# Kernel optimization log

Measured on AMD Instinct MI355X. Metric: run time of the kernel, lower is better.

## Reference

```python
import jax, jax.numpy as jnp
import numpy as np

EPS_SUM = 1e-8   # matches tf divide epsilon on column sums
EPS_L2 = 1e-12   # tf.nn.l2_normalize default epsilon inside CosineSimilarity
EPS_LOG = 1e-8


def _l2norm_rows(x):
    # rows: (k, N); matches tf.nn.l2_normalize(x, axis=-1)
    sq = jnp.sum(x * x, axis=-1, keepdims=True)
    return x * jax.lax.rsqrt(jnp.maximum(sq, EPS_L2))


def setup_inputs() -> dict:
    key = jax.random.key(0)
    k0, k1 = jax.random.split(key)
    N, K = 200000, 256
    c_0 = jax.random.uniform(k0, (N, K), dtype=jnp.float32)
    c_1 = jax.random.uniform(k1, (N, K), dtype=jnp.float32)
    return {"c_0": c_0, "c_1": c_1, "k": K}


def reference(c_0, c_1, k):
    # --- cluster-size entropy terms ---
    s0 = jnp.sum(c_0, axis=0)                      # (k,)
    s1 = jnp.sum(c_1, axis=0)
    p_0 = s0 / jnp.sum(s0)
    p_1 = s1 / jnp.sum(s1)
    log_k = jnp.log(jnp.float32(k))
    entrpy_loss = (jnp.sum(p_0 * jnp.log(p_0)) + log_k) + \
                  (jnp.sum(p_1 * jnp.log(p_1)) + log_k)

    # --- column-sum normalize, transpose to (k, N) ---
    c0n = (c_0 / (s0[None, :] + EPS_SUM)).T        # (k, N)
    c1n = (c_1 / (s1[None, :] + EPS_SUM)).T        # (k, N)

    # cosine similarity matrix via row L2-normalization + small GEMM
    a = _l2norm_rows(c0n)                          # (k, N)
    b = _l2norm_rows(c1n)                          # (k, N)
    c_smi = jnp.einsum('kn,jn->kj', a, b)          # (k, k) cosine sims

    diag = jnp.diagonal(jax.nn.softmax(c_smi, axis=-1))  # (k,)
    cls_loss = -jnp.mean(jnp.log(diag + EPS_LOG))
    return (cls_loss, entrpy_loss)
```

## Files before the change

kernel.cpp:

```cpp
#include <hip/hip_runtime.h>
#include <hip/hip_bf16.h>

typedef __attribute__((ext_vector_type(4))) float f32x4;
typedef __attribute__((ext_vector_type(4))) int   i32x4;
typedef __attribute__((ext_vector_type(8))) short s16x8;

#define KCOLS 256
#define KC 32

__device__ __forceinline__ unsigned int f2bf(float v){
    union { float f; unsigned int u; } x; x.f = v;
    return (x.u + 0x7fffu + ((x.u >> 16) & 1u)) >> 16;
}

__global__ __launch_bounds__(512, 2) void k1_gemm(
        const float* __restrict__ c0, const float* __restrict__ c1,
        float* __restrict__ Pc, float* __restrict__ Ps, int nrows)
{
    const int tid = threadIdx.x;
    const int w   = tid >> 6;
    const int l   = tid & 63;
    const int mat = w >> 2;
    const int oct = w & 3;
    const int wr  = w >> 2;
    const int wc  = w & 3;
    const int b   = blockIdx.x;
    const int B   = gridDim.x;
    const int nchunk = (nrows + KC - 1) / KC;

    __shared__ __align__(16) unsigned short lds[2][2][8192];
    __shared__ float sred[2][4][256];
    __shared__ float qred[2][4][256];

    const float* src = mat ? c1 : c0;
    const int colbase = l << 2;
    const int wsw = ((oct ^ (l & 3)) << 3);

    int idxA[8], idxB[4];
#pragma unroll
    for (int mt = 0; mt < 8; ++mt){
        int col = wr*128 + mt*16 + (l & 15);
        idxA[mt] = col*32 + ((((l >> 4)) ^ ((col >> 2) & 3)) << 3);
    }
#pragma unroll
    for (int nt = 0; nt < 4; ++nt){
        int col = wc*64 + nt*16 + (l & 15);
        idxB[nt] = col*32 + ((((l >> 4)) ^ ((col >> 2) & 3)) << 3);
    }

    f32x4 acc[8][4];
    const f32x4 zf = {0.f, 0.f, 0.f, 0.f};
#pragma unroll
    for (int i = 0; i < 8; ++i)
#pragma unroll
        for (int j = 0; j < 4; ++j) acc[i][j] = zf;

    float sum[4] = {0.f,0.f,0.f,0.f};
    float sq [4] = {0.f,0.f,0.f,0.f};

    f32x4 f[8];
    int c = b;
    if (c < nchunk){
        int rbase = c*KC + oct*8;
#pragma unroll
        for (int rr = 0; rr < 8; ++rr){
            int row = rbase + rr;
            f[rr] = (row < nrows) ? *(const f32x4*)(src + (size_t)row*KCOLS + colbase) : zf;
        }
    }

    int p = 0;
    while (c < nchunk){
        unsigned short* dst = &lds[p][mat][0];
#pragma unroll
        for (int cc = 0; cc < 4; ++cc){
            float v0=f[0][cc], v1=f[1][cc], v2=f[2][cc], v3=f[3][cc];
            float v4=f[4][cc], v5=f[5][cc], v6=f[6][cc], v7=f[7][cc];
            sum[cc] += ((v0+v1)+(v2+v3)) + ((v4+v5)+(v6+v7));
            sq [cc] += ((v0*v0+v1*v1)+(v2*v2+v3*v3)) + ((v4*v4+v5*v5)+(v6*v6+v7*v7));
            i32x4 pk;
            pk.x = (int)(f2bf(v0) | (f2bf(v1) << 16));
            pk.y = (int)(f2bf(v2) | (f2bf(v3) << 16));
            pk.z = (int)(f2bf(v4) | (f2bf(v5) << 16));
            pk.w = (int)(f2bf(v6) | (f2bf(v7) << 16));
            *(i32x4*)&dst[(colbase + cc)*32 + wsw] = pk;
        }
        __syncthreads();

        int cn = c + B;
        if (cn < nchunk){
            int rbase = cn*KC + oct*8;
#pragma unroll
            for (int rr = 0; rr < 8; ++rr){
                int row = rbase + rr;
                f[rr] = (row < nrows) ? *(const f32x4*)(src + (size_t)row*KCOLS + colbase) : zf;
            }
        }

        const unsigned short* bufA = &lds[p][0][0];
        const unsigned short* bufB = &lds[p][1][0];
        s16x8 bfr[4];
#pragma unroll
        for (int nt = 0; nt < 4; ++nt) bfr[nt] = *(const s16x8*)&bufB[idxB[nt]];
#pragma unroll
        for (int mt = 0; mt < 8; ++mt){
            s16x8 afr = *(const s16x8*)&bufA[idxA[mt]];
#pragma unroll
            for (int nt = 0; nt < 4; ++nt)
                acc[mt][nt] = __builtin_amdgcn_mfma_f32_16x16x32_bf16(
                                  afr, bfr[nt], acc[mt][nt], 0, 0, 0);
        }
        p ^= 1;
        c  = cn;
    }

    float* Pb = Pc + (size_t)b * 65536;
#pragma unroll
    for (int mt = 0; mt < 8; ++mt)
#pragma unroll
        for (int nt = 0; nt < 4; ++nt)
#pragma unroll
            for (int r = 0; r < 4; ++r){
                int row = wr*128 + mt*16 + (l >> 4)*4 + r;
                int cl  = wc*64  + nt*16 + (l & 15);
                Pb[row*256 + cl] = acc[mt][nt][r];
            }

#pragma unroll
    for (int cc = 0; cc < 4; ++cc){
        sred[mat][oct][colbase + cc] = sum[cc];
        qred[mat][oct][colbase + cc] = sq[cc];
    }
    __syncthreads();
    {
        int m2 = tid >> 8, cl = tid & 255;
        float s = sred[m2][0][cl] + sred[m2][1][cl] + sred[m2][2][cl] + sred[m2][3][cl];
        float q = qred[m2][0][cl] + qred[m2][1][cl] + qred[m2][2][cl] + qred[m2][3][cl];
        Ps[(size_t)b*1024 + m2*512 + cl]       = s;
        Ps[(size_t)b*1024 + m2*512 + 256 + cl] = q;
    }
}

__global__ __launch_bounds__(256) void k2_sum(const float* __restrict__ Ps,
                                              float* __restrict__ fin, int B)
{
    int tid = threadIdx.x;
    int u   = blockIdx.x*64 + (tid & 63);
    int sub = tid >> 6;
    double a = 0.0;
    for (int b = sub; b < B; b += 4) a += Ps[(size_t)b*1024 + u];
    __shared__ double sc2[4][64];
    sc2[sub][tid & 63] = a;
    __syncthreads();
    if (sub == 0)
        fin[u] = (float)(sc2[0][tid] + sc2[1][tid] + sc2[2][tid] + sc2[3][tid]);
}

__global__ __launch_bounds__(512) void k3_rows(const float* __restrict__ Pc,
        const float* __restrict__ fin, float* __restrict__ tout, int B)
{
    const int j   = blockIdx.x;
    const int tid = threadIdx.x;
    const int l   = tid & 255;
    const int h   = tid >> 8;

    __shared__ float part[2][256];
    __shared__ float cosS[256];
    __shared__ float wred[8];

    double a = 0.0;
    int b0 = h ? (B >> 1) : 0;
    int b1 = h ? B        : (B >> 1);
    for (int b = b0; b < b1; ++b)
        a += Pc[(size_t)b*65536 + j*256 + l];
    part[h][l] = (float)a;
    __syncthreads();

    if (h == 0){
        float Cjl = part[0][l] + part[1][l];
        float d0 = fin[j]       + 1e-8f, q0 = fin[256 + j];
        float d1 = fin[512 + l] + 1e-8f, q1 = fin[768 + l];
        float rs0 = rsqrtf(fmaxf(q0 / (d0*d0), 1e-12f));
        float rs1 = rsqrtf(fmaxf(q1 / (d1*d1), 1e-12f));
        cosS[l] = Cjl * (rs0 / d0) * (rs1 / d1);
    }
    __syncthreads();

    float v  = (tid < 256) ? cosS[tid] : -3.0e38f;
    float mx = v;
#pragma unroll
    for (int o = 32; o >= 1; o >>= 1) mx = fmaxf(mx, __shfl_xor(mx, o));
    if ((tid & 63) == 0) wred[tid >> 6] = mx;
    __syncthreads();
    mx = wred[0];
#pragma unroll
    for (int i = 1; i < 8; ++i) mx = fmaxf(mx, wred[i]);
    __syncthreads();

    float e = (tid < 256) ? expf(cosS[tid] - mx) : 0.0f;
    float s = e;
#pragma unroll
    for (int o = 32; o >= 1; o >>= 1) s += __shfl_xor(s, o);
    if ((tid & 63) == 0) wred[tid >> 6] = s;
    __syncthreads();
    float S = ((wred[0]+wred[1])+(wred[2]+wred[3])) + ((wred[4]+wred[5])+(wred[6]+wred[7]));

    if (tid == j){
        float dg = expf(cosS[j] - mx) / S;
        tout[j] = logf(dg + 1e-8f);
    }
}

__global__ __launch_bounds__(256) void k4_fin(const float* __restrict__ fin,
        const float* __restrict__ tout, const int* __restrict__ kptr,
        float* __restrict__ out)
{
    const int tid = threadIdx.x;
    __shared__ double sc[4];
    auto bsum = [&](double v) -> double {
#pragma unroll
        for (int o = 32; o >= 1; o >>= 1) v += __shfl_xor(v, o);
        if ((tid & 63) == 0) sc[tid >> 6] = v;
        __syncthreads();
        double r = sc[0] + sc[1] + sc[2] + sc[3];
        __syncthreads();
        return r;
    };

    double s0 = fin[tid], s1 = fin[512 + tid];
    double S0 = bsum(s0), S1 = bsum(s1);
    double p0 = s0 / S0, p1 = s1 / S1;
    double T0 = bsum(p0 * log(p0));
    double T1 = bsum(p1 * log(p1));
    double Tc = bsum((double)tout[tid]);

    if (tid == 0){
        double lk = log((double)(*kptr));
        out[0] = (float)(-(Tc / 256.0));
        out[1] = (float)((T0 + lk) + (T1 + lk));
    }
}

extern "C" void kernel_launch(void* const* d_in, const int* in_sizes, int n_in,
                              void* d_out, int out_size, void* d_ws, size_t ws_size,
                              hipStream_t stream)
{
    const float* c0  = (const float*)d_in[0];
    const float* c1  = (const float*)d_in[1];
    const int*  kptr = (const int*)d_in[2];
    float* out = (float*)d_out;
    int nrows = in_sizes[0] / KCOLS;

    int B = 256;
    size_t need = ((size_t)B*66560 + 1280) * sizeof(float);
    if (need > ws_size){
        long cap = (long)(ws_size / sizeof(float)) - 1280;
        long bb  = cap / 66560;
        B = (int)(bb < 1 ? 1 : (bb > 256 ? 256 : bb));
    }
    float* Pc  = (float*)d_ws;
    float* Ps  = Pc + (size_t)B * 65536;
    float* fin = Ps + (size_t)B * 1024;
    float* tv  = fin + 1024;

    hipLaunchKernelGGL(k1_gemm, dim3(B),   dim3(512), 0, stream, c0, c1, Pc, Ps, nrows);
    hipLaunchKernelGGL(k2_sum,  dim3(16),  dim3(256), 0, stream, Ps, fin, B);
    hipLaunchKernelGGL(k3_rows, dim3(256), dim3(512), 0, stream, Pc, fin, tv, B);
    hipLaunchKernelGGL(k4_fin,  dim3(1),   dim3(256), 0, stream, fin, tv, kptr, out);
}
```

Measured before the change: 146.6 us.

## Use hardware bf16 pack, new LDS swizzle, custom barrier, and even grid

Replaces software bf16 rounding with the v_cvt_pk_bf16_f32 instruction and changes the LDS swizzle to an 8-way XOR layout for both writes and MFMA fragment reads. The next chunk's global load is now issued before a custom barrier that waits only on LDS counters, so the global loads can overlap the barrier and the MFMA phase. A fast path skips per-row bounds checks, and the grid changes to 250 blocks so the 6250 chunks divide evenly. Moving the barrier relies on the double-buffered LDS staying race-free with the new ordering.

```diff
diff --git a/kernel.cpp b/kernel.cpp
--- a/kernel.cpp
+++ b/kernel.cpp
@@ -8,9 +8,22 @@
 #define KCOLS 256
 #define KC 32
 
-__device__ __forceinline__ unsigned int f2bf(float v){
-    union { float f; unsigned int u; } x; x.f = v;
-    return (x.u + 0x7fffu + ((x.u >> 16) & 1u)) >> 16;
+__device__ __forceinline__ int swz_idx(int col, int koct){
+    return ((col >> 1) << 6) + ((((((col & 1) << 2) | koct)) ^ ((col >> 2) & 7)) << 3);
+}
+
+__device__ __forceinline__ int cvt2(float lo, float hi){
+    int r;
+    asm("v_cvt_pk_bf16_f32 %0, %1, %2" : "=v"(r) : "v"(lo), "v"(hi));
+    return r;
+}
+
+__device__ __forceinline__ void block_barrier(){
+    asm volatile("s_waitcnt lgkmcnt(0)" ::: "memory");
+    __builtin_amdgcn_sched_barrier(0);
+    __builtin_amdgcn_s_barrier();
+    __builtin_amdgcn_sched_barrier(0);
+    asm volatile("" ::: "memory");
 }
 
 __global__ __launch_bounds__(512, 2) void k1_gemm(
@@ -34,19 +47,20 @@
 
     const float* src = mat ? c1 : c0;
     const int colbase = l << 2;
-    const int wsw = ((oct ^ (l & 3)) << 3);
 
     int idxA[8], idxB[4];
 #pragma unroll
-    for (int mt = 0; mt < 8; ++mt){
-        int col = wr*128 + mt*16 + (l & 15);
-        idxA[mt] = col*32 + ((((l >> 4)) ^ ((col >> 2) & 3)) << 3);
-    }
-#pragma unroll
-    for (int nt = 0; nt < 4; ++nt){
-        int col = wc*64 + nt*16 + (l & 15);
-        idxB[nt] = col*32 + ((((l >> 4)) ^ ((col >> 2) & 3)) << 3);
-    }
+    for (int mt = 0; mt < 8; ++mt)
+        idxA[mt] = swz_idx(wr*128 + mt*16 + (l & 15), l >> 4);
+#pragma unroll
+    for (int nt = 0; nt < 4; ++nt)
+        idxB[nt] = swz_idx(wc*64 + nt*16 + (l & 15), l >> 4);
+
+    int widx[4];
+#pragma unroll
+    for (int cc = 0; cc < 4; ++cc)
+        widx[cc] = (((l << 1) + (cc >> 1)) << 6) +
+                   ((((((cc & 1) << 2) | oct)) ^ (l & 7)) << 3);
 
     f32x4 acc[8][4];
     const f32x4 zf = {0.f, 0.f, 0.f, 0.f};
@@ -59,16 +73,23 @@
     float sq [4] = {0.f,0.f,0.f,0.f};
 
     f32x4 f[8];
+    auto LOAD = [&](int c){
+        int rbase = c*KC + oct*8;
+        if (rbase + 8 <= nrows){
+#pragma unroll
+            for (int rr = 0; rr < 8; ++rr)
+                f[rr] = *(const f32x4*)(src + (size_t)(rbase+rr)*KCOLS + colbase);
+        } else {
+#pragma unroll
+            for (int rr = 0; rr < 8; ++rr){
+                int row = rbase + rr;
+                f[rr] = (row < nrows) ? *(const f32x4*)(src + (size_t)row*KCOLS + colbase) : zf;
+            }
+        }
+    };
+
     int c = b;
-    if (c < nchunk){
-        int rbase = c*KC + oct*8;
-#pragma unroll
-        for (int rr = 0; rr < 8; ++rr){
-            int row = rbase + rr;
-            f[rr] = (row < nrows) ? *(const f32x4*)(src + (size_t)row*KCOLS + colbase) : zf;
-        }
-    }
-
+    if (c < nchunk) LOAD(c);
     int p = 0;
     while (c < nchunk){
         unsigned short* dst = &lds[p][mat][0];
@@ -79,23 +100,17 @@
             sum[cc] += ((v0+v1)+(v2+v3)) + ((v4+v5)+(v6+v7));
             sq [cc] += ((v0*v0+v1*v1)+(v2*v2+v3*v3)) + ((v4*v4+v5*v5)+(v6*v6+v7*v7));
             i32x4 pk;
-            pk.x = (int)(f2bf(v0) | (f2bf(v1) << 16));
-            pk.y = (int)(f2bf(v2) | (f2bf(v3) << 16));
-            pk.z = (int)(f2bf(v4) | (f2bf(v5) << 16));
-            pk.w = (int)(f2bf(v6) | (f2bf(v7) << 16));
-            *(i32x4*)&dst[(colbase + cc)*32 + wsw] = pk;
+            pk.x = cvt2(v0, v1);
+            pk.y = cvt2(v2, v3);
+            pk.z = cvt2(v4, v5);
+            pk.w = cvt2(v6, v7);
+            *(i32x4*)&dst[widx[cc]] = pk;
         }
-        __syncthreads();
 
         int cn = c + B;
-        if (cn < nchunk){
-            int rbase = cn*KC + oct*8;
-#pragma unroll
-            for (int rr = 0; rr < 8; ++rr){
-                int row = rbase + rr;
-                f[rr] = (row < nrows) ? *(const f32x4*)(src + (size_t)row*KCOLS + colbase) : zf;
-            }
-        }
+        if (cn < nchunk) LOAD(cn);
+
+        block_barrier();
 
         const unsigned short* bufA = &lds[p][0][0];
         const unsigned short* bufB = &lds[p][1][0];
@@ -251,12 +266,12 @@
     float* out = (float*)d_out;
     int nrows = in_sizes[0] / KCOLS;
 
-    int B = 256;
+    int B = 250;
     size_t need = ((size_t)B*66560 + 1280) * sizeof(float);
     if (need > ws_size){
         long cap = (long)(ws_size / sizeof(float)) - 1280;
         long bb  = cap / 66560;
-        B = (int)(bb < 1 ? 1 : (bb > 256 ? 256 : bb));
+        B = (int)(bb < 1 ? 1 : (bb > 250 ? 250 : bb));
     }
     float* Pc  = (float*)d_ws;
     float* Ps  = Pc + (size_t)B * 65536;
```

Measured after the change: 144.8 us. Within noise of the previous version (-1.3%).
